# Kernel tuning notes

Measured on AMD Instinct MI355X. Metric: run time of the kernel, lower is better.

## Reference

```python
import jax, jax.numpy as jnp
import numpy as np

J = 50
HEADS = 4
DIMS = [3, 64, 128, 256]
POSE_DIM = 512
B, T = 16, 128


def build_edge_index():
    # 49-bone chain over 50 joints, symmetrized, plus self-loops
    # (PyG GATConv adds self-loops by default).
    e = []
    for i in range(J - 1):
        e.append((i, i + 1))
        e.append((i + 1, i))
    for i in range(J):
        e.append((i, i))
    e = sorted(e)
    return jnp.array(e, dtype=jnp.int32).T  # [2, E]


def setup_inputs() -> dict:
    key = jax.random.key(0)
    ks = iter(jax.random.split(key, 64))
    def nrm(shape, s):
        return jax.random.normal(next(ks), shape, jnp.float32) * s
    inp = {"pose_seq": jax.random.normal(next(ks), (B, T, J, 3), jnp.float32)}
    for i in range(3):
        din, dout = DIMS[i], DIMS[i + 1]
        C = dout // HEADS
        inp[f"W{i}"] = nrm((din, dout), din ** -0.5)        # GATConv lin (no bias)
        inp[f"as{i}"] = nrm((HEADS, C), 0.1)                 # att_src
        inp[f"ad{i}"] = nrm((HEADS, C), 0.1)                 # att_dst
        inp[f"bg{i}"] = jnp.zeros((dout,), jnp.float32)      # GATConv bias
        inp[f"R{i}"] = nrm((din, dout), din ** -0.5)         # residual Linear (no bias)
        inp[f"g{i}"] = jnp.ones((dout,), jnp.float32)        # LayerNorm gamma
        inp[f"b{i}"] = jnp.zeros((dout,), jnp.float32)       # LayerNorm beta
    inp["fpW"] = nrm((J * DIMS[-1], POSE_DIM), (J * DIMS[-1]) ** -0.5)
    inp["fpb"] = jnp.zeros((POSE_DIM,), jnp.float32)
    inp["fng"] = jnp.ones((POSE_DIM,), jnp.float32)
    inp["fnb"] = jnp.zeros((POSE_DIM,), jnp.float32)
    inp["edge_index"] = build_edge_index()
    return inp


def _layer_norm(x, g, b, eps=1e-5):
    mu = jnp.mean(x, axis=-1, keepdims=True)
    var = jnp.mean(jnp.square(x - mu), axis=-1, keepdims=True)
    return (x - mu) * jax.lax.rsqrt(var + eps) * g + b


def _gat(x, src, dst, W, a_s, a_d, bias):
    # x: [G, J, Fin]; edges identical across the G graphs.
    G, Jn, _ = x.shape
    H, C = a_s.shape
    h = (x @ W).reshape(G, Jn, H, C)
    es = jnp.einsum('gjhc,hc->gjh', h, a_s)[:, src]   # [G,E,H]
    ed = jnp.einsum('gjhc,hc->gjh', h, a_d)[:, dst]
    e = jax.nn.leaky_relu(es + ed, 0.2)
    # per-destination softmax over incoming edges (per head)
    m = jnp.full((G, Jn, H), -jnp.inf, e.dtype).at[:, dst].max(e)
    m = jax.lax.stop_gradient(m)
    w = jnp.exp(e - m[:, dst])
    den = jnp.zeros((G, Jn, H), e.dtype).at[:, dst].add(w)
    alpha = w / den[:, dst]                            # [G,E,H]
    out = jnp.zeros((G, Jn, H, C), e.dtype).at[:, dst].add(alpha[..., None] * h[:, src])
    return out.reshape(G, Jn, H * C) + bias


def _forward(pose_seq, layers, fpW, fpb, fng, fnb, edge_index):
    Bb, Tt = pose_seq.shape[0], pose_seq.shape[1]
    x = pose_seq.reshape(Bb * Tt, J, 3)
    src, dst = edge_index[0], edge_index[1]
    for (W, a_s, a_d, bg, R, g, b) in layers:
        h = _gat(x, src, dst, W, a_s, a_d, bg)
        res = x @ R  # dims always change -> Linear residual (bias=False)
        x = jax.nn.gelu(_layer_norm(h + res, g, b), approximate=False)
    x = x.reshape(Bb * Tt, J * DIMS[-1]) @ fpW + fpb
    x = _layer_norm(x, fng, fnb)
    return x.reshape(Bb, Tt, POSE_DIM)


def reference(pose_seq, W0, as0, ad0, bg0, R0, g0, b0,
              W1, as1, ad1, bg1, R1, g1, b1,
              W2, as2, ad2, bg2, R2, g2, b2,
              fpW, fpb, fng, fnb, edge_index):
    layers = [(W0, as0, ad0, bg0, R0, g0, b0),
              (W1, as1, ad1, bg1, R1, g1, b1),
              (W2, as2, ad2, bg2, R2, g2, b2)]
    return _forward(pose_seq, layers, fpW, fpb, fng, fnb, edge_index)
```

## Files before the change

kernel.cpp:

```cpp
#include <hip/hip_runtime.h>
#include <hip/hip_bf16.h>
#include <math.h>

#define J 50
#define GN 2048
#define GK 12800
#define GON 512

#define SPLITK 8
#define BKC (GK / SPLITK)
#define NKT (BKC / 64)

typedef short short8 __attribute__((ext_vector_type(8)));
typedef float f32x4 __attribute__((ext_vector_type(4)));

__device__ __forceinline__ float lrelu(float x) { return x > 0.f ? x : 0.2f * x; }
__device__ __forceinline__ ushort f2bu(float f) { __hip_bfloat16 h = __float2bfloat16(f); return *(ushort*)&h; }

__device__ __forceinline__ float gelu_fast(float y) {
    float u = y * (1.f + 0.044715f * y * y);
    float t = __expf(-1.5957691216f * u);
    return y * __builtin_amdgcn_rcpf(1.f + t);
}

__device__ __forceinline__ float dpp_sum16(float s) {
    int v;
    v = __builtin_amdgcn_update_dpp(0, __builtin_bit_cast(int, s), 0x128, 0xF, 0xF, true);
    s += __builtin_bit_cast(float, v);
    v = __builtin_amdgcn_update_dpp(0, __builtin_bit_cast(int, s), 0x124, 0xF, 0xF, true);
    s += __builtin_bit_cast(float, v);
    v = __builtin_amdgcn_update_dpp(0, __builtin_bit_cast(int, s), 0x122, 0xF, 0xF, true);
    s += __builtin_bit_cast(float, v);
    v = __builtin_amdgcn_update_dpp(0, __builtin_bit_cast(int, s), 0x121, 0xF, 0xF, true);
    s += __builtin_bit_cast(float, v);
    return s;
}


template<int DIN, int KPAD, int DOUT, bool LAST>
__device__ __forceinline__ void gat_layer_v3(
    int tid, ushort* xbf, float* esW, float* Acoef, float* statsC, float* statsN,
    const ushort* __restrict__ Wt, const ushort* __restrict__ Rt,
    const ushort* __restrict__ Wex,
    const float* __restrict__ bg, const float* __restrict__ gam,
    const float* __restrict__ bet, ushort* __restrict__ gout)
{
    constexpr int NFW = DOUT / 64;
    constexpr int GRX = KPAD / 8;
    constexpr int XM  = (GRX < 8 ? GRX : 8) - 1;
    constexpr int NKS = KPAD / 32;
    const int lane = tid & 63, w = tid >> 6;
    const int lr = lane & 15, lg = lane >> 4;

    f32x4 acc[4][NFW];
    f32x4 ext[4];

    #pragma unroll
    for (int m = 0; m < 4; ++m) {
        ext[m] = (f32x4){0.f, 0.f, 0.f, 0.f};
        #pragma unroll
        for (int nf = 0; nf < NFW; ++nf) acc[m][nf] = (f32x4){0.f, 0.f, 0.f, 0.f};
    }
    #pragma unroll
    for (int ks = 0; ks < NKS; ++ks) {
        short8 af[4];
        #pragma unroll
        for (int m = 0; m < 4; ++m) {
            int row = m * 16 + lr;
            int g = (ks * 4 + lg) ^ (row & XM);
            af[m] = *(const short8*)&xbf[(row * GRX + g) * 8];
        }
        __builtin_amdgcn_s_setprio(1);
        #pragma unroll
        for (int nf = 0; nf < NFW; ++nf) {
            int col = (w * NFW + nf) * 16 + lr;
            short8 bf = *(const short8*)&Wt[col * KPAD + ks * 32 + lg * 8];
            #pragma unroll
            for (int m = 0; m < 4; ++m)
                acc[m][nf] = __builtin_amdgcn_mfma_f32_16x16x32_bf16(af[m], bf, acc[m][nf], 0, 0, 0);
        }
        short8 bfe = *(const short8*)&Wex[(w * 16 + lr) * KPAD + ks * 32 + lg * 8];
        #pragma unroll
        for (int m = 0; m < 4; ++m)
            ext[m] = __builtin_amdgcn_mfma_f32_16x16x32_bf16(af[m], bfe, ext[m], 0, 0, 0);
        __builtin_amdgcn_s_setprio(0);
    }

    if (lr < 2) {
        float* dstp = &esW[w * 130 + lr * 65];
        #pragma unroll
        for (int m = 0; m < 4; ++m)
            #pragma unroll
            for (int q = 0; q < 4; ++q)
                dstp[m * 16 + lg * 4 + q] = ext[m][q];
    }
    asm volatile("s_waitcnt lgkmcnt(0)" ::: "memory");

    {
        int r = lane;
        const float* ew = &esW[w * 130];
        float es0 = ew[r];
        float esm = ew[r > 0 ? r - 1 : 0];
        float esp = ew[r < 63 ? r + 1 : 63];
        float edj = ew[65 + r];
        float e1 = lrelu(es0 + edj);
        float e0 = (r > 0)     ? lrelu(esm + edj) : -1e30f;
        float e2 = (r < J - 1) ? lrelu(esp + edj) : -1e30f;
        float mx = fmaxf(e1, fmaxf(e0, e2));
        float w0 = __expf(e0 - mx), w1 = __expf(e1 - mx), w2 = __expf(e2 - mx);
        float rden = 1.f / (w0 + w1 + w2);
        Acoef[w * 192 + r]       = w0 * rden;
        Acoef[w * 192 + 64 + r]  = w1 * rden;
        Acoef[w * 192 + 128 + r] = w2 * rden;
    }
    asm volatile("s_waitcnt lgkmcnt(0)" ::: "memory");

    #pragma unroll
    for (int nf = 0; nf < NFW; ++nf) {
        float rp[4], rn[4];
        #pragma unroll
        for (int m = 0; m < 4; ++m) {
            rp[m] = __shfl(acc[m][nf][3], (lane + 48) & 63);
            rn[m] = __shfl(acc[m][nf][0], (lane + 16) & 63);
        }
        float tmp[4][4];
        #pragma unroll
        for (int m = 0; m < 4; ++m) {
            int rb = m * 16 + lg * 4;
            float4 c0 = *(const float4*)&Acoef[w * 192 + rb];
            float4 c1 = *(const float4*)&Acoef[w * 192 + 64 + rb];
            float4 c2 = *(const float4*)&Acoef[w * 192 + 128 + rb];
            int mp = m > 0 ? m - 1 : 0, mn = m < 3 ? m + 1 : 3;
            float hprev = (lg > 0) ? rp[m] : rp[mp];
            float hnext = (lg < 3) ? rn[m] : rn[mn];
            tmp[m][0] = c0.x * hprev         + c1.x * acc[m][nf][0] + c2.x * acc[m][nf][1];
            tmp[m][1] = c0.y * acc[m][nf][0] + c1.y * acc[m][nf][1] + c2.y * acc[m][nf][2];
            tmp[m][2] = c0.z * acc[m][nf][1] + c1.z * acc[m][nf][2] + c2.z * acc[m][nf][3];
            tmp[m][3] = c0.w * acc[m][nf][2] + c1.w * acc[m][nf][3] + c2.w * hnext;
        }
        #pragma unroll
        for (int m = 0; m < 4; ++m)
            #pragma unroll
            for (int q = 0; q < 4; ++q) acc[m][nf][q] = tmp[m][q];
    }

    #pragma unroll
    for (int ks = 0; ks < NKS; ++ks) {
        short8 af[4];
        #pragma unroll
        for (int m = 0; m < 4; ++m) {
            int row = m * 16 + lr;
            int g = (ks * 4 + lg) ^ (row & XM);
            af[m] = *(const short8*)&xbf[(row * GRX + g) * 8];
        }
        __builtin_amdgcn_s_setprio(1);
        #pragma unroll
        for (int nf = 0; nf < NFW; ++nf) {
            int col = (w * NFW + nf) * 16 + lr;
            short8 bf = *(const short8*)&Rt[col * KPAD + ks * 32 + lg * 8];
            #pragma unroll
            for (int m = 0; m < 4; ++m)
                acc[m][nf] = __builtin_amdgcn_mfma_f32_16x16x32_bf16(af[m], bf, acc[m][nf], 0, 0, 0);
        }
        __builtin_amdgcn_s_setprio(0);
    }
    #pragma unroll
    for (int nf = 0; nf < NFW; ++nf) {
        float bgv = bg[(w * NFW + nf) * 16 + lr];
        #pragma unroll
        for (int m = 0; m < 4; ++m)
            #pragma unroll
            for (int q = 0; q < 4; ++q) acc[m][nf][q] += bgv;
    }

    #pragma unroll
    for (int m = 0; m < 4; ++m)
        #pragma unroll
        for (int q = 0; q < 4; ++q) {
            float s = 0.f, s2 = 0.f;
            #pragma unroll
            for (int nf = 0; nf < NFW; ++nf) {
                float v = acc[m][nf][q];
                s += v; s2 += v * v;
            }
            s  = dpp_sum16(s);
            s2 = dpp_sum16(s2);
            if (lr == 0) {
                int row = m * 16 + lg * 4 + q;
                atomicAdd(&statsC[row * 2], s);
                atomicAdd(&statsC[row * 2 + 1], s2);
            }
        }
    __syncthreads();

    constexpr int NGR = DOUT / 8;
    constexpr int NXM = (NGR < 8 ? NGR : 8) - 1;
    {
        float gav[NFW], bev[NFW];
        #pragma unroll
        for (int nf = 0; nf < NFW; ++nf) {
            int col = (w * NFW + nf) * 16 + lr;
            gav[nf] = gam[col]; bev[nf] = bet[col];
        }
        #pragma unroll
        for (int m = 0; m < 4; ++m)
            #pragma unroll
            for (int q = 0; q < 4; ++q) {
                int row = m * 16 + lg * 4 + q;
                float S = statsC[row * 2], S2 = statsC[row * 2 + 1];
                float mu = S * (1.f / DOUT);
                float inv = rsqrtf(fmaf(S2, 1.f / DOUT, -mu * mu) + 1e-5f);
                float miv = -mu * inv;
                #pragma unroll
                for (int nf = 0; nf < NFW; ++nf) {
                    int col = (w * NFW + nf) * 16 + lr;
                    float y = fmaf(acc[m][nf][q], inv, miv);
                    y = fmaf(y, gav[nf], bev[nf]);
                    float ge = gelu_fast(y);
                    if (LAST) {
                        if (row < J) gout[row * 256 + col] = f2bu(ge);
                    } else {
                        xbf[(row * NGR + ((col >> 3) ^ (row & NXM))) * 8 + (col & 7)] =
                            (row < J) ? f2bu(ge) : (ushort)0;
                    }
                }
            }
    }
    if (tid < 128) statsN[tid] = 0.f;
    __syncthreads();
}

__global__ __launch_bounds__(256, 4) void gat_mfma(
    const float* __restrict__ pose,
    const ushort* __restrict__ Wt0, const ushort* __restrict__ Rt0,
    const ushort* __restrict__ Wt1, const ushort* __restrict__ Rt1,
    const ushort* __restrict__ Wt2, const ushort* __restrict__ Rt2,
    const ushort* __restrict__ wex0, const ushort* __restrict__ wex1,
    const ushort* __restrict__ wex2,
    const float* bg0, const float* g0v, const float* b0v,
    const float* bg1, const float* g1v, const float* b1v,
    const float* bg2, const float* g2v, const float* b2v,
    ushort* __restrict__ xg)
{
    __shared__ ushort xbf[64 * 128];
    __shared__ float esW[4 * 130];
    __shared__ float Acoef[4 * 192];
    __shared__ float sA[128], sB[128];
    int g = blockIdx.x, tid = threadIdx.x;

    for (int i = tid; i < 64 * 32; i += 256) {
        int row = i >> 5, c = i & 31;
        float v = (row < J && c < 3) ? pose[(size_t)g * (J * 3) + row * 3 + c] : 0.f;
        xbf[(row * 4 + ((c >> 3) ^ (row & 3))) * 8 + (c & 7)] = f2bu(v);
    }
    if (tid < 128) sA[tid] = 0.f;
    __syncthreads();
    gat_layer_v3<3,   32,  64, false>(tid, xbf, esW, Acoef, sA, sB, Wt0, Rt0, wex0,
                                      bg0, g0v, b0v, nullptr);
    gat_layer_v3<64,  64, 128, false>(tid, xbf, esW, Acoef, sB, sA, Wt1, Rt1, wex1,
                                      bg1, g1v, b1v, nullptr);
    gat_layer_v3<128,128, 256, true >(tid, xbf, esW, Acoef, sA, sB, Wt2, Rt2, wex2,
                                      bg2, g2v, b2v, xg + (size_t)g * GK);
}

__global__ __launch_bounds__(256) void prep_all(
    const float* __restrict__ W0, const float* __restrict__ R0,
    const float* __restrict__ W1, const float* __restrict__ R1,
    const float* __restrict__ W2, const float* __restrict__ R2,
    const float* __restrict__ as0, const float* __restrict__ ad0,
    const float* __restrict__ as1, const float* __restrict__ ad1,
    const float* __restrict__ as2, const float* __restrict__ ad2,
    const float* __restrict__ fpW,
    ushort* __restrict__ wt, ushort* __restrict__ wex, ushort* __restrict__ Bt)
{
    __shared__ float tile[64][65];
    int bid = blockIdx.x, tid = threadIdx.x;
    if (bid < 336) {
        int i = bid * 256 + tid;
        if (i < 2048)       { int n = i >> 5, k = i & 31;                    wt[i] = f2bu(k < 3 ? W0[k * 64 + n] : 0.f); }
        else if (i < 4096)  { int j = i - 2048;  int n = j >> 5, k = j & 31; wt[i] = f2bu(k < 3 ? R0[k * 64 + n] : 0.f); }
        else if (i < 12288) { int j = i - 4096;  int n = j >> 6, k = j & 63; wt[i] = f2bu(W1[k * 128 + n]); }
        else if (i < 20480) { int j = i - 12288; int n = j >> 6, k = j & 63; wt[i] = f2bu(R1[k * 128 + n]); }
        else if (i < 53248) { int j = i - 20480; int n = j >> 7, k = j & 127; wt[i] = f2bu(W2[k * 256 + n]); }
        else if (i < 86016) { int j = i - 53248; int n = j >> 7, k = j & 127; wt[i] = f2bu(R2[k * 256 + n]); }
    } else if (bid < 392) {
        int i = (bid - 336) * 256 + tid;
        const float *as_, *ad_, *W; ushort* dst; int KPAD, DIN, DOUT, idx;
        if (i < 2048)       { idx = i;         KPAD = 32;  DIN = 3;   DOUT = 64;  as_ = as0; ad_ = ad0; W = W0; dst = wex; }
        else if (i < 6144)  { idx = i - 2048;  KPAD = 64;  DIN = 64;  DOUT = 128; as_ = as1; ad_ = ad1; W = W1; dst = wex + 2048; }
        else if (i < 14336) { idx = i - 6144;  KPAD = 128; DIN = 128; DOUT = 256; as_ = as2; ad_ = ad2; W = W2; dst = wex + 6144; }
        else return;
        int k = idx % KPAD;
        int col = (idx / KPAD) & 15;
        int h = idx / (KPAD * 16);
        int C = DOUT / 4;
        float v = 0.f;
        if (col < 2 && k < DIN) {
            const float* a = (col == 0) ? as_ : ad_;
            for (int c = 0; c < C; ++c) v += W[k * DOUT + h * C + c] * a[h * C + c];
        }
        dst[idx] = f2bu(v);
    } else {
        int b = bid - 392;
        int kb = (b >> 3) * 64;
        int nb = (b & 7) * 64;
        #pragma unroll
        for (int i = 0; i < 16; ++i) {
            int idx = tid + i * 256;
            int r = idx >> 6, c = idx & 63;
            tile[r][c] = fpW[(size_t)(kb + r) * GON + nb + c];
        }
        __syncthreads();
        #pragma unroll
        for (int i = 0; i < 16; ++i) {
            int idx = tid + i * 256;
            int nr = idx >> 6, kc = idx & 63;
            Bt[(size_t)(nb + nr) * GK + kb + kc] = f2bu(tile[kc][nr]);
        }
    }
}

__global__ __launch_bounds__(512) void final_gemm_mfma(
    const ushort* __restrict__ A,
    const ushort* __restrict__ Bt,
    float* __restrict__ parts)
{
    __shared__ ushort Asm[2][128 * 64];
    __shared__ ushort Bsm[2][128 * 64];
    int tid = threadIdx.x;
    int bid = blockIdx.x;
    int tileid = bid & 63, sp = bid >> 6;
    int rt = tileid >> 2, ct = tileid & 3;
    int ar0 = rt * 128, bc0 = ct * 128;
    int kbase = sp * BKC;

    int lane = tid & 63, wid = tid >> 6;
    int wm = wid >> 2, wn = wid & 3;

    f32x4 acc[4][2];
    #pragma unroll
    for (int mi = 0; mi < 4; ++mi)
        #pragma unroll
        for (int ni = 0; ni < 2; ++ni)
            acc[mi][ni] = (f32x4){0.f, 0.f, 0.f, 0.f};

#define STAGE(pg, k0)                                                              \
    do {                                                                           \
        _Pragma("unroll")                                                          \
        for (int s_ = 0; s_ < 4; ++s_) {                                           \
            int g_ = tid + s_ * 512;                                               \
            int gg_ = g_ & 1023;                                                   \
            int row_ = gg_ >> 3, cg_ = gg_ & 7;                                    \
            int csw_ = cg_ ^ (row_ & 7);                                           \
            const ushort* src_;                                                    \
            ushort* dst_;                                                          \
            if (g_ < 1024) {                                                       \
                src_ = A + (size_t)(ar0 + row_) * GK + (k0) + csw_ * 8;            \
                dst_ = &Asm[pg][gg_ * 8];                                          \
            } else {                                                               \
                src_ = Bt + (size_t)(bc0 + row_) * GK + (k0) + csw_ * 8;           \
                dst_ = &Bsm[pg][gg_ * 8];                                          \
            }                                                                      \
            __builtin_amdgcn_global_load_lds(                                      \
                (const __attribute__((address_space(1))) void*)src_,               \
                (__attribute__((address_space(3))) void*)dst_, 16, 0, 0);          \
        }                                                                          \
    } while (0)

    STAGE(0, kbase);
    __syncthreads();
    int pg = 0;
    for (int kt = 0; kt < NKT; ++kt) {
        if (kt + 1 < NKT) STAGE(pg ^ 1, kbase + (kt + 1) * 64);
        const ushort* Ab = Asm[pg];
        const ushort* Bb = Bsm[pg];
        short8 afr[4][2], bfr[2][2];
        #pragma unroll
        for (int mi = 0; mi < 4; ++mi)
            #pragma unroll
            for (int ks = 0; ks < 2; ++ks) {
                int row = wm * 64 + mi * 16 + (lane & 15);
                int gs = (ks * 4 + (lane >> 4)) ^ (row & 7);
                afr[mi][ks] = *(const short8*)&Ab[row * 64 + gs * 8];
            }
        #pragma unroll
        for (int ni = 0; ni < 2; ++ni)
            #pragma unroll
            for (int ks = 0; ks < 2; ++ks) {
                int row = wn * 32 + ni * 16 + (lane & 15);
                int gs = (ks * 4 + (lane >> 4)) ^ (row & 7);
                bfr[ni][ks] = *(const short8*)&Bb[row * 64 + gs * 8];
            }
        #pragma unroll
        for (int ks = 0; ks < 2; ++ks)
            #pragma unroll
            for (int mi = 0; mi < 4; ++mi)
                #pragma unroll
                for (int ni = 0; ni < 2; ++ni)
                    acc[mi][ni] = __builtin_amdgcn_mfma_f32_16x16x32_bf16(
                        afr[mi][ks], bfr[ni][ks], acc[mi][ni], 0, 0, 0);
        __syncthreads();
        pg ^= 1;
    }
#undef STAGE

    float* outp = parts + (size_t)sp * GN * GON;
    #pragma unroll
    for (int mi = 0; mi < 4; ++mi)
        #pragma unroll
        for (int ni = 0; ni < 2; ++ni)
            #pragma unroll
            for (int r = 0; r < 4; ++r) {
                int row = ar0 + wm * 64 + mi * 16 + (lane >> 4) * 4 + r;
                int col = bc0 + wn * 32 + ni * 16 + (lane & 15);
                outp[(size_t)row * GON + col] = acc[mi][ni][r];
            }
}

__global__ __launch_bounds__(256) void final_reduce_ln(
    const float* __restrict__ parts, float* __restrict__ out,
    const float* __restrict__ fpb, const float* __restrict__ fng,
    const float* __restrict__ fnb)
{
    int row = blockIdx.x * 4 + (threadIdx.x >> 6);
    int lane = threadIdx.x & 63;
    float v[8];
    float sum = 0.f;
    #pragma unroll
    for (int cc = 0; cc < 8; ++cc) {
        int o = lane + (cc << 6);
        float a = 0.f;
        #pragma unroll
        for (int s = 0; s < SPLITK; ++s)
            a += parts[(size_t)s * GN * GON + (size_t)row * GON + o];
        v[cc] = a + fpb[o];
        sum += v[cc];
    }
    #pragma unroll
    for (int off = 32; off >= 1; off >>= 1) sum += __shfl_xor(sum, off, 64);
    float mu = sum * (1.f / GON);
    float sq = 0.f;
    #pragma unroll
    for (int cc = 0; cc < 8; ++cc) { float d = v[cc] - mu; sq += d * d; }
    #pragma unroll
    for (int off = 32; off >= 1; off >>= 1) sq += __shfl_xor(sq, off, 64);
    float inv = rsqrtf(sq * (1.f / GON) + 1e-5f);
    #pragma unroll
    for (int cc = 0; cc < 8; ++cc) {
        int o = lane + (cc << 6);
        out[(size_t)row * GON + o] = (v[cc] - mu) * inv * fng[o] + fnb[o];
    }
}

extern "C" void kernel_launch(void* const* d_in, const int* in_sizes, int n_in,
                              void* d_out, int out_size, void* d_ws, size_t ws_size,
                              hipStream_t stream) {
    (void)in_sizes; (void)n_in; (void)out_size; (void)ws_size;
    const float* pose = (const float*)d_in[0];
    const float *W0 = (const float*)d_in[1],  *as0 = (const float*)d_in[2],
                *ad0 = (const float*)d_in[3], *bg0 = (const float*)d_in[4],
                *R0 = (const float*)d_in[5],  *g0v = (const float*)d_in[6],
                *b0v = (const float*)d_in[7];
    const float *W1 = (const float*)d_in[8],  *as1 = (const float*)d_in[9],
                *ad1 = (const float*)d_in[10],*bg1 = (const float*)d_in[11],
                *R1 = (const float*)d_in[12], *g1v = (const float*)d_in[13],
                *b1v = (const float*)d_in[14];
    const float *W2 = (const float*)d_in[15], *as2 = (const float*)d_in[16],
                *ad2 = (const float*)d_in[17],*bg2 = (const float*)d_in[18],
                *R2 = (const float*)d_in[19], *g2v = (const float*)d_in[20],
                *b2v = (const float*)d_in[21];
    const float* fpW = (const float*)d_in[22];
    const float* fpb = (const float*)d_in[23];
    const float* fng = (const float*)d_in[24];
    const float* fnb = (const float*)d_in[25];

    ushort* xg = (ushort*)d_ws;
    ushort* Bt = xg + (size_t)GN * GK;
    float* parts = (float*)(Bt + (size_t)GON * GK);
    ushort* wsm = (ushort*)(parts + (size_t)SPLITK * GN * GON);
    ushort *Wt0 = wsm,          *Rt0 = wsm + 2048;
    ushort *Wt1 = wsm + 4096,   *Rt1 = wsm + 12288;
    ushort *Wt2 = wsm + 20480,  *Rt2 = wsm + 53248;
    ushort* wex = wsm + 86016;
    ushort *wex0 = wex, *wex1 = wex + 2048, *wex2 = wex + 6144;
    float* out = (float*)d_out;

    prep_all<<<392 + (GK / 64) * (GON / 64), 256, 0, stream>>>(
        W0, R0, W1, R1, W2, R2,
        as0, ad0, as1, ad1, as2, ad2,
        fpW, wsm, wex, Bt);
    gat_mfma<<<GN, 256, 0, stream>>>(pose,
        Wt0, Rt0, Wt1, Rt1, Wt2, Rt2,
        wex0, wex1, wex2,
        bg0, g0v, b0v,
        bg1, g1v, b1v,
        bg2, g2v, b2v, xg);
    final_gemm_mfma<<<64 * SPLITK, 512, 0, stream>>>(xg, Bt, parts);
    final_reduce_ln<<<GN / 4, 256, 0, stream>>>(parts, out, fpb, fng, fnb);
}
```

Before: 158.0 us.

## Fold fpW transpose into GAT kernel blocks to overlap with GAT compute

```diff
diff --git a/kernel.cpp b/kernel.cpp
--- a/kernel.cpp
+++ b/kernel.cpp
@@ -10,6 +10,8 @@
 #define SPLITK 8
 #define BKC (GK / SPLITK)
 #define NKT (BKC / 64)
+
+#define NTB ((GK / 64) * (GON / 64))
 
 typedef short short8 __attribute__((ext_vector_type(8)));
 typedef float f32x4 __attribute__((ext_vector_type(4)));
@@ -240,13 +242,38 @@
     const float* bg0, const float* g0v, const float* b0v,
     const float* bg1, const float* g1v, const float* b1v,
     const float* bg2, const float* g2v, const float* b2v,
+    const float* __restrict__ fpW, ushort* __restrict__ Bt,
     ushort* __restrict__ xg)
 {
-    __shared__ ushort xbf[64 * 128];
-    __shared__ float esW[4 * 130];
-    __shared__ float Acoef[4 * 192];
-    __shared__ float sA[128], sB[128];
+    __shared__ __align__(16) char smem[22560];
     int g = blockIdx.x, tid = threadIdx.x;
+
+    if (g >= GN) {
+        float* tile = (float*)smem;
+        int b = g - GN;
+        int kb = (b >> 3) * 64;
+        int nb = (b & 7) * 64;
+        #pragma unroll
+        for (int i = 0; i < 16; ++i) {
+            int idx = tid + i * 256;
+            int r = idx >> 6, c = idx & 63;
+            tile[r * 65 + c] = fpW[(size_t)(kb + r) * GON + nb + c];
+        }
+        __syncthreads();
+        #pragma unroll
+        for (int i = 0; i < 16; ++i) {
+            int idx = tid + i * 256;
+            int nr = idx >> 6, kc = idx & 63;
+            Bt[(size_t)(nb + nr) * GK + kb + kc] = f2bu(tile[kc * 65 + nr]);
+        }
+        return;
+    }
+
+    ushort* xbf  = (ushort*)smem;
+    float*  esW  = (float*)(smem + 16384);
+    float*  Acoef= (float*)(smem + 16384 + 2080);
+    float*  sA   = (float*)(smem + 16384 + 2080 + 3072);
+    float*  sB   = sA + 128;
 
     for (int i = tid; i < 64 * 32; i += 256) {
         int row = i >> 5, c = i & 31;
@@ -263,17 +290,15 @@
                                       bg2, g2v, b2v, xg + (size_t)g * GK);
 }
 
-__global__ __launch_bounds__(256) void prep_all(
+__global__ __launch_bounds__(256) void prep_small(
     const float* __restrict__ W0, const float* __restrict__ R0,
     const float* __restrict__ W1, const float* __restrict__ R1,
     const float* __restrict__ W2, const float* __restrict__ R2,
     const float* __restrict__ as0, const float* __restrict__ ad0,
     const float* __restrict__ as1, const float* __restrict__ ad1,
     const float* __restrict__ as2, const float* __restrict__ ad2,
-    const float* __restrict__ fpW,
-    ushort* __restrict__ wt, ushort* __restrict__ wex, ushort* __restrict__ Bt)
+    ushort* __restrict__ wt, ushort* __restrict__ wex)
 {
-    __shared__ float tile[64][65];
     int bid = blockIdx.x, tid = threadIdx.x;
     if (bid < 336) {
         int i = bid * 256 + tid;
@@ -283,7 +308,7 @@
         else if (i < 20480) { int j = i - 12288; int n = j >> 6, k = j & 63; wt[i] = f2bu(R1[k * 128 + n]); }
         else if (i < 53248) { int j = i - 20480; int n = j >> 7, k = j & 127; wt[i] = f2bu(W2[k * 256 + n]); }
         else if (i < 86016) { int j = i - 53248; int n = j >> 7, k = j & 127; wt[i] = f2bu(R2[k * 256 + n]); }
-    } else if (bid < 392) {
+    } else {
         int i = (bid - 336) * 256 + tid;
         const float *as_, *ad_, *W; ushort* dst; int KPAD, DIN, DOUT, idx;
         if (i < 2048)       { idx = i;         KPAD = 32;  DIN = 3;   DOUT = 64;  as_ = as0; ad_ = ad0; W = W0; dst = wex; }
@@ -300,23 +325,6 @@
             for (int c = 0; c < C; ++c) v += W[k * DOUT + h * C + c] * a[h * C + c];
         }
         dst[idx] = f2bu(v);
-    } else {
-        int b = bid - 392;
-        int kb = (b >> 3) * 64;
-        int nb = (b & 7) * 64;
-        #pragma unroll
-        for (int i = 0; i < 16; ++i) {
-            int idx = tid + i * 256;
-            int r = idx >> 6, c = idx & 63;
-            tile[r][c] = fpW[(size_t)(kb + r) * GON + nb + c];
-        }
-        __syncthreads();
-        #pragma unroll
-        for (int i = 0; i < 16; ++i) {
-            int idx = tid + i * 256;
-            int nr = idx >> 6, kc = idx & 63;
-            Bt[(size_t)(nb + nr) * GK + kb + kc] = f2bu(tile[kc][nr]);
-        }
     }
 }
 
@@ -485,16 +493,16 @@
     ushort *wex0 = wex, *wex1 = wex + 2048, *wex2 = wex + 6144;
     float* out = (float*)d_out;
 
-    prep_all<<<392 + (GK / 64) * (GON / 64), 256, 0, stream>>>(
+    prep_small<<<392, 256, 0, stream>>>(
         W0, R0, W1, R1, W2, R2,
-        as0, ad0, as1, ad1, as2, ad2,
-        fpW, wsm, wex, Bt);
-    gat_mfma<<<GN, 256, 0, stream>>>(pose,
+        as0, ad0, as1, ad1, as2, ad2, wsm, wex);
+    gat_mfma<<<GN + NTB, 256, 0, stream>>>(pose,
         Wt0, Rt0, Wt1, Rt1, Wt2, Rt2,
         wex0, wex1, wex2,
         bg0, g0v, b0v,
         bg1, g1v, b1v,
-        bg2, g2v, b2v, xg);
+        bg2, g2v, b2v,
+        fpW, Bt, xg);
     final_gemm_mfma<<<64 * SPLITK, 512, 0, stream>>>(xg, Bt, parts);
     final_reduce_ln<<<GN / 4, 256, 0, stream>>>(parts, out, fpb, fng, fnb);
 }
```

Measured after the change: 162.3 us. 1.03x slower.
